# Optimization experiments

Hardware: AMD Instinct MI355X
Metric: run time of the kernel (lower is better)

The kernel has to match this reference:

```python
import jax, jax.numpy as jnp
import numpy as np

N_USER = 100000
N_SELLER = 50000
E = 640000
D_U = 128
D_S = 64
H = 128
B = 50000


def setup_inputs() -> dict:
    key = jax.random.key(0)
    ks = jax.random.split(key, 24)

    def w(k, shape):
        # Glorot-ish scaling by fan_in
        return jax.random.normal(k, shape, dtype=jnp.float32) / np.sqrt(shape[0])

    return {
        "x_user": jax.random.normal(ks[0], (N_USER, D_U), dtype=jnp.float32),
        "x_seller": jax.random.normal(ks[1], (N_SELLER, D_S), dtype=jnp.float32),
        "src_buy": jax.random.randint(ks[2], (E,), 0, N_USER),
        "dst_buy": jax.random.randint(ks[3], (E,), 0, N_SELLER),
        "src_rev": jax.random.randint(ks[4], (E,), 0, N_SELLER),
        "dst_rev": jax.random.randint(ks[5], (E,), 0, N_USER),
        "mask_user": jax.random.randint(ks[6], (B,), 0, N_USER),
        "mask_seller": jax.random.randint(ks[7], (B,), 0, N_SELLER),
        # layer 1: (user,buy,seller) conv: src=user(D_U), dst=seller(D_S)
        "Wl1_buy": w(ks[8], (D_U, H)), "Wr1_buy": w(ks[9], (D_S, H)),
        "b1_buy": jnp.zeros((H,), jnp.float32),
        # layer 1: (seller,bought by,user) conv: src=seller(D_S), dst=user(D_U)
        "Wl1_rev": w(ks[10], (D_S, H)), "Wr1_rev": w(ks[11], (D_U, H)),
        "b1_rev": jnp.zeros((H,), jnp.float32),
        # layer 2 (both node types now have H features)
        "Wl2_buy": w(ks[12], (H, H)), "Wr2_buy": w(ks[13], (H, H)),
        "b2_buy": jnp.zeros((H,), jnp.float32),
        "Wl2_rev": w(ks[14], (H, H)), "Wr2_rev": w(ks[15], (H, H)),
        "b2_rev": jnp.zeros((H,), jnp.float32),
        # final head: Linear(2H, 1)
        "Wlin": w(ks[16], (2 * H, 1)), "blin": jnp.zeros((1,), jnp.float32),
    }


def _sage(x_src, x_dst, src, dst, Wl, Wr, b):
    """PyG SAGEConv: lin_l(mean_j x_src[j]) + lin_r(x_dst); bias on aggr branch."""
    n_dst = x_dst.shape[0]
    agg = jax.ops.segment_sum(x_src[src], dst, num_segments=n_dst)      # [n_dst, d_src]
    cnt = jax.ops.segment_sum(jnp.ones(src.shape, x_src.dtype), dst, num_segments=n_dst)
    mean = agg / jnp.maximum(cnt, 1.0)[:, None]                          # mean aggr, 0 for isolated
    return mean @ Wl + b + x_dst @ Wr


def reference(x_user, x_seller, src_buy, dst_buy, src_rev, dst_rev,
              mask_user, mask_seller,
              Wl1_buy, Wr1_buy, b1_buy, Wl1_rev, Wr1_rev, b1_rev,
              Wl2_buy, Wr2_buy, b2_buy, Wl2_rev, Wr2_rev, b2_rev,
              Wlin, blin):
    # layer 1 (HeteroConv aggr='sum' is trivial: one relation per dst type)
    s1 = jax.nn.relu(_sage(x_user, x_seller, src_buy, dst_buy, Wl1_buy, Wr1_buy, b1_buy))
    u1 = jax.nn.relu(_sage(x_seller, x_user, src_rev, dst_rev, Wl1_rev, Wr1_rev, b1_rev))
    # layer 2
    s2 = jax.nn.relu(_sage(u1, s1, src_buy, dst_buy, Wl2_buy, Wr2_buy, b2_buy))
    u2 = jax.nn.relu(_sage(s1, u1, src_rev, dst_rev, Wl2_rev, Wr2_rev, b2_rev))
    # masked gather + concat + linear + sigmoid
    x = jnp.concatenate((u2[mask_user], s2[mask_seller]), axis=1)        # [B, 2H]
    return jax.nn.sigmoid(x @ Wlin + blin).reshape(-1)
```

## Files before the change

kernel.cpp:

```cpp
#include <hip/hip_runtime.h>

#define N_USER   100000
#define N_SELLER 50000
#define NEDGE    640000
#define DU       128
#define DS       64
#define HH       128
#define BSZ      50000

#define ECHUNK   2048
#define NBLK     313
#define PW       128
#define NPART_B  391
#define NPART_R  782

#define CVT_BLK  15625
#define PREP_BLK 448

#define NB1_BUY  391
#define NB1_REV  782
#define NB2      391

#define AGG1_BUY_BLK 12500
#define AGG1_REV_BLK 25000
#define AGG2_BLK     12500

typedef unsigned short ushort_t;
typedef __attribute__((ext_vector_type(4))) unsigned short u16x4;
typedef __attribute__((ext_vector_type(8))) unsigned short u16x8;
typedef __attribute__((ext_vector_type(8))) short bf16x8;
typedef __attribute__((ext_vector_type(4))) float f32x4;

__device__ __forceinline__ float bf2f(ushort_t u) {
  union { unsigned int i; float f; } v; v.i = ((unsigned int)u) << 16; return v.f;
}
__device__ __forceinline__ ushort_t f2bf(float f) {
  union { float f; unsigned int i; } v; v.f = f;
  unsigned int x = v.i;
  unsigned int r = x + 0x7FFFu + ((x >> 16) & 1u);
  return (ushort_t)(r >> 16);
}

__global__ void __launch_bounds__(256) k_hist_cvt_prep(
    const int* __restrict__ dst_buy, const int* __restrict__ dst_rev,
    int* __restrict__ H_buy, int* __restrict__ H_rev,
    const float* __restrict__ x_user, ushort_t* __restrict__ xu_bf,
    const float* __restrict__ x_seller, ushort_t* __restrict__ xs_bf,
    const float* __restrict__ Wl1b, const float* __restrict__ Wr1b, ushort_t* __restrict__ o1b,
    const float* __restrict__ Wl1r, const float* __restrict__ Wr1r, ushort_t* __restrict__ o1r,
    const float* __restrict__ Wl2b, const float* __restrict__ Wr2b, ushort_t* __restrict__ o2b,
    const float* __restrict__ Wl2r, const float* __restrict__ Wr2r, ushort_t* __restrict__ o2r) {
  __shared__ int lh[NPART_R];
  int b = blockIdx.x;
  int t = threadIdx.x;
  if (b < 2 * NBLK) {
    bool is_buy = b < NBLK;
    int bb = is_buy ? b : b - NBLK;
    const int* dst = is_buy ? dst_buy : dst_rev;
    int* H = is_buy ? H_buy : H_rev;
    int np = is_buy ? NPART_B : NPART_R;
    for (int i = t; i < np; i += 256) lh[i] = 0;
    __syncthreads();
    int base = bb * ECHUNK;
#pragma unroll
    for (int i = 0; i < 8; ++i) {
      int e = base + i * 256 + t;
      if (e < NEDGE) atomicAdd(&lh[dst[e] >> 7], 1);
    }
    __syncthreads();
    for (int p = t; p < np; p += 256) H[p * NBLK + bb] = lh[p];
  } else if (b < 2 * NBLK + CVT_BLK) {
    int idx = (b - 2 * NBLK) * 256 + t;
    const int na4 = N_USER * DU / 4;
    const float* in; ushort_t* out;
    if (idx < na4) { in = x_user + idx * 4; out = xu_bf + idx * 4; }
    else { idx -= na4; in = x_seller + idx * 4; out = xs_bf + idx * 4; }
    float4 v = *(const float4*)in;
    u16x4 r;
    r.x = f2bf(v.x); r.y = f2bf(v.y); r.z = f2bf(v.z); r.w = f2bf(v.w);
    *(u16x4*)out = r;
  } else {
    int idx = (b - 2 * NBLK - CVT_BLK) * 256 + t;
    const float *Wl, *Wr; ushort_t* out; int D1;
    if (idx < 24576)      { Wl = Wl1b; Wr = Wr1b; out = o1b; D1 = 128; }
    else if (idx < 49152) { idx -= 24576; Wl = Wl1r; Wr = Wr1r; out = o1r; D1 = 64; }
    else if (idx < 81920) { idx -= 49152; Wl = Wl2b; Wr = Wr2b; out = o2b; D1 = 128; }
    else                  { idx -= 81920; Wl = Wl2r; Wr = Wr2r; out = o2r; D1 = 128; }
    int f = idx >> 9;
    int r = idx & 511;
    int l = r >> 3;
    int j = r & 7;
    int kcidx = f >> 3;
    int c = f & 7;
    int h = (l & 15) + c * 16;
    int k = kcidx * 32 + (l >> 4) * 8 + j;
    float w = (k < D1) ? Wl[k * HH + h] : Wr[(k - D1) * HH + h];
    out[idx] = f2bf(w);
  }
}

__global__ void __launch_bounds__(256) k_rowscan(
    int* __restrict__ H_buy, int* __restrict__ H_rev,
    int* __restrict__ rowtot_buy, int* __restrict__ rowtot_rev) {
  __shared__ int lds[256];
  int p = blockIdx.x, t = threadIdx.x;
  int* H; int* rowtot; int row;
  if (p < NPART_B) { H = H_buy; rowtot = rowtot_buy; row = p; }
  else             { H = H_rev; rowtot = rowtot_rev; row = p - NPART_B; }
  int i0 = 2 * t, i1 = 2 * t + 1;
  int v0 = (i0 < NBLK) ? H[row * NBLK + i0] : 0;
  int v1 = (i1 < NBLK) ? H[row * NBLK + i1] : 0;
  int tot = v0 + v1;
  lds[t] = tot;
  __syncthreads();
  for (int d = 1; d < 256; d <<= 1) {
    int x = (t >= d) ? lds[t - d] : 0;
    __syncthreads();
    lds[t] += x;
    __syncthreads();
  }
  int excl = lds[t] - tot;
  if (i0 < NBLK) H[row * NBLK + i0] = excl;
  if (i1 < NBLK) H[row * NBLK + i1] = excl + v0;
  if (t == 255) rowtot[row] = lds[255];
}

__global__ void __launch_bounds__(256) k_colscan(
    const int* __restrict__ rowtot_buy, const int* __restrict__ rowtot_rev,
    int* __restrict__ pstart_buy, int* __restrict__ pstart_rev) {
  __shared__ int lds[256];
  const int* rt; int* ps; int n;
  if (blockIdx.x == 0) { rt = rowtot_buy; ps = pstart_buy; n = NPART_B; }
  else                 { rt = rowtot_rev; ps = pstart_rev; n = NPART_R; }
  int t = threadIdx.x;
  int v[4]; int tot = 0;
#pragma unroll
  for (int i = 0; i < 4; ++i) { int idx = t * 4 + i; v[i] = (idx < n) ? rt[idx] : 0; tot += v[i]; }
  lds[t] = tot;
  __syncthreads();
  for (int d = 1; d < 256; d <<= 1) {
    int x = (t >= d) ? lds[t - d] : 0;
    __syncthreads();
    lds[t] += x;
    __syncthreads();
  }
  int excl = lds[t] - tot;
#pragma unroll
  for (int i = 0; i < 4; ++i) {
    int idx = t * 4 + i;
    if (idx < n) { ps[idx] = excl; excl += v[i]; }
  }
  if (t == 255) ps[n] = lds[255];
}

__global__ void __launch_bounds__(256) k_pscat(
    const int* __restrict__ src_buy, const int* __restrict__ dst_buy,
    const int* __restrict__ src_rev, const int* __restrict__ dst_rev,
    const int* __restrict__ H_buy, const int* __restrict__ H_rev,
    const int* __restrict__ pstart_buy, const int* __restrict__ pstart_rev,
    unsigned int* __restrict__ part_buy, unsigned int* __restrict__ part_rev) {
  __shared__ int lc[NPART_R];
  int b = blockIdx.x, t = threadIdx.x;
  bool is_buy = b < NBLK;
  int bb = is_buy ? b : b - NBLK;
  const int* src = is_buy ? src_buy : src_rev;
  const int* dst = is_buy ? dst_buy : dst_rev;
  const int* H   = is_buy ? H_buy : H_rev;
  const int* ps  = is_buy ? pstart_buy : pstart_rev;
  unsigned int* part = is_buy ? part_buy : part_rev;
  int np = is_buy ? NPART_B : NPART_R;
  for (int i = t; i < np; i += 256) lc[i] = 0;
  __syncthreads();
  int base = bb * ECHUNK;
#pragma unroll
  for (int i = 0; i < 8; ++i) {
    int e = base + i * 256 + t;
    if (e < NEDGE) {
      int d = dst[e], s = src[e];
      int p = d >> 7;
      int r = atomicAdd(&lc[p], 1);
      int pos = ps[p] + H[p * NBLK + bb] + r;
      part[pos] = ((unsigned int)(d & (PW - 1)) << 20) | (unsigned int)s;
    }
  }
}

__global__ void __launch_bounds__(256) k_csr(
    const unsigned int* __restrict__ part_buy, const unsigned int* __restrict__ part_rev,
    const int* __restrict__ pstart_buy, const int* __restrict__ pstart_rev,
    int* __restrict__ off_buy, int* __restrict__ off_rev,
    int* __restrict__ csr_buy, int* __restrict__ csr_rev) {
  __shared__ int lcnt[PW], loff[PW], sc[PW];
  int B = blockIdx.x, t = threadIdx.x;
  bool is_buy = B < NPART_B;
  int p = is_buy ? B : B - NPART_B;
  const unsigned int* part = is_buy ? part_buy : part_rev;
  const int* ps = is_buy ? pstart_buy : pstart_rev;
  int* off = is_buy ? off_buy : off_rev;
  int* csr = is_buy ? csr_buy : csr_rev;
  int nnode = is_buy ? N_SELLER : N_USER;
  int s0 = ps[p], s1 = ps[p + 1];
  if (t < PW) lcnt[t] = 0;
  __syncthreads();
  for (int e = s0 + t; e < s1; e += 256) {
    int d = (int)(part[e] >> 20);
    atomicAdd(&lcnt[d], 1);
  }
  __syncthreads();
  int v = (t < PW) ? lcnt[t] : 0;
  if (t < PW) sc[t] = v;
  __syncthreads();
  for (int d = 1; d < PW; d <<= 1) {
    int x = (t >= d && t < PW) ? sc[t - d] : 0;
    __syncthreads();
    if (t < PW) sc[t] += x;
    __syncthreads();
  }
  if (t < PW) {
    loff[t] = sc[t] - v;
    int node = p * PW + t;
    if (node < nnode) off[node] = s0 + loff[t];
    lcnt[t] = 0;
  }
  if (B == 0 && t == 0) { off_buy[N_SELLER] = NEDGE; off_rev[N_USER] = NEDGE; }
  __syncthreads();
  for (int e = s0 + t; e < s1; e += 256) {
    unsigned int pk = part[e];
    int l = (int)(pk >> 20);
    int r = atomicAdd(&lcnt[l], 1);
    csr[s0 + loff[l] + r] = (int)(pk & 0xFFFFFu);
  }
}

template <int D, int U>
__device__ __forceinline__ void agg_body(
    int blk, const ushort_t* __restrict__ X,
    const int* __restrict__ off, const int* __restrict__ csr,
    const int* __restrict__ idxs, int nrows,
    ushort_t* __restrict__ out) {
  constexpr int LPR = D / 8;
  constexpr int EPW = 64 / LPR;
  int wave = threadIdx.x >> 6;
  int lane = threadIdx.x & 63;
  int n = blk * 4 + wave;
  if (n >= nrows) return;
  int node = idxs ? idxs[n] : n;
  int g = lane / LPR;
  int c = (lane % LPR) * 8;
  int i0 = off[node], i1 = off[node + 1];

  float acc[8];
#pragma unroll
  for (int j = 0; j < 8; ++j) acc[j] = 0.f;

  for (int i = i0 + g; i < i1; i += U * EPW) {
    int idx[U];
    u16x8 v[U];
#pragma unroll
    for (int u = 0; u < U; ++u) {
      int ii = i + u * EPW;
      idx[u] = (ii < i1) ? csr[ii] : csr[i];
    }
#pragma unroll
    for (int u = 0; u < U; ++u)
      v[u] = *(const u16x8*)(X + (size_t)idx[u] * D + c);
#pragma unroll
    for (int u = 0; u < U; ++u) {
      if (i + u * EPW < i1) {
#pragma unroll
        for (int j = 0; j < 8; ++j) acc[j] += bf2f(v[u][j]);
      }
    }
  }

#pragma unroll
  for (int mm = LPR; mm < 64; mm <<= 1) {
#pragma unroll
    for (int j = 0; j < 8; ++j) acc[j] += __shfl_xor(acc[j], mm);
  }

  if (g == 0) {
    int deg = i1 - i0;
    float inv = 1.f / (float)(deg > 0 ? deg : 1);
    u16x8 r;
#pragma unroll
    for (int j = 0; j < 8; ++j) r[j] = f2bf(acc[j] * inv);
    *(u16x8*)(out + (size_t)n * D + c) = r;
  }
}

__global__ void __launch_bounds__(256) agg_layer1(
    const ushort_t* __restrict__ xu_bf, const ushort_t* __restrict__ xs_bf,
    const int* __restrict__ off_buy, const int* __restrict__ csr_buy,
    const int* __restrict__ off_rev, const int* __restrict__ csr_rev,
    ushort_t* __restrict__ mean_buy, ushort_t* __restrict__ mean_rev) {
  int b = blockIdx.x;
  if (b < AGG1_BUY_BLK)
    agg_body<128, 4>(b, xu_bf, off_buy, csr_buy, nullptr, N_SELLER, mean_buy);
  else
    agg_body<64, 2>(b - AGG1_BUY_BLK, xs_bf, off_rev, csr_rev, nullptr, N_USER, mean_rev);
}

__global__ void __launch_bounds__(256) agg_layer2(
    const ushort_t* __restrict__ u1, const ushort_t* __restrict__ s1,
    const int* __restrict__ off_buy, const int* __restrict__ csr_buy,
    const int* __restrict__ off_rev, const int* __restrict__ csr_rev,
    const int* __restrict__ mask_seller, const int* __restrict__ mask_user,
    ushort_t* __restrict__ mean_buy, ushort_t* __restrict__ mean_rev) {
  int b = blockIdx.x;
  if (b < AGG2_BLK)
    agg_body<128, 4>(b, u1, off_buy, csr_buy, mask_seller, BSZ, mean_buy);
  else
    agg_body<128, 4>(b - AGG2_BLK, s1, off_rev, csr_rev, mask_user, BSZ, mean_rev);
}

template <int K, bool HEAD>
__device__ __forceinline__ void gemm_body(
    int blk, ushort_t* lds,
    const ushort_t* __restrict__ A1, int ld1, int D1, const int* __restrict__ mask1,
    const ushort_t* __restrict__ A2, int ld2, const int* __restrict__ mask2,
    const ushort_t* __restrict__ Wf, const float* __restrict__ bias,
    ushort_t* __restrict__ out, float* __restrict__ partial,
    const float* __restrict__ wlin_seg, int M) {
  constexpr int NCH = K / 32;
  int t = threadIdx.x;
  int wave = t >> 6;
  int lane = t & 63;

  constexpr int ITERS = (HH * K * 2) / 4096;
#pragma unroll
  for (int i = 0; i < ITERS; ++i) {
    const ushort_t* g = Wf + i * 2048 + t * 8;
    ushort_t* l = lds + i * 2048 + wave * 512;
    __builtin_amdgcn_global_load_lds((const __attribute__((address_space(1))) void*)g,
                                     (__attribute__((address_space(3))) void*)l, 16, 0, 0);
  }

  int row0 = blk * 128 + wave * 32;
  int kb = (lane >> 4) << 3;
  bf16x8 af[2][NCH];
#pragma unroll
  for (int s = 0; s < 2; ++s) {
    int r = row0 + s * 16 + (lane & 15);
    int rsafe = r < M ? r : M - 1;
    int a1 = mask1 ? mask1[rsafe] : rsafe;
    int a2 = mask2 ? mask2[rsafe] : rsafe;
#pragma unroll
    for (int kc = 0; kc < NCH; ++kc) {
      int k = kc * 32 + kb;
      const ushort_t* ap = (k < D1) ? (A1 + (size_t)a1 * ld1 + k)
                                    : (A2 + (size_t)a2 * ld2 + (k - D1));
      af[s][kc] = *(const bf16x8*)ap;
    }
  }

  f32x4 acc[2][8];
#pragma unroll
  for (int s = 0; s < 2; ++s)
#pragma unroll
    for (int c = 0; c < 8; ++c) acc[s][c] = (f32x4){0.f, 0.f, 0.f, 0.f};

  __syncthreads();

#pragma unroll
  for (int kc = 0; kc < NCH; ++kc) {
#pragma unroll
    for (int c = 0; c < 8; ++c) {
      bf16x8 bf = *(const bf16x8*)(lds + ((kc * 8 + c) * 512 + lane * 8));
      acc[0][c] = __builtin_amdgcn_mfma_f32_16x16x32_bf16(af[0][kc], bf, acc[0][c], 0, 0, 0);
      acc[1][c] = __builtin_amdgcn_mfma_f32_16x16x32_bf16(af[1][kc], bf, acc[1][c], 0, 0, 0);
    }
  }

  int colb = lane & 15;
  if constexpr (!HEAD) {
#pragma unroll
    for (int s = 0; s < 2; ++s) {
      int rbase = row0 + s * 16 + ((lane >> 4) << 2);
#pragma unroll
      for (int c = 0; c < 8; ++c) {
        int col = c * 16 + colb;
        float bv = bias[col];
#pragma unroll
        for (int j = 0; j < 4; ++j) {
          int rout = rbase + j;
          if (rout < M) {
            float v = fmaxf(acc[s][c][j] + bv, 0.f);
            out[(size_t)rout * HH + col] = f2bf(v);
          }
        }
      }
    }
  } else {
    float wl[8], bv[8];
#pragma unroll
    for (int c = 0; c < 8; ++c) {
      wl[c] = wlin_seg[c * 16 + colb];
      bv[c] = bias[c * 16 + colb];
    }
#pragma unroll
    for (int s = 0; s < 2; ++s) {
      float p0 = 0.f, p1 = 0.f, p2 = 0.f, p3 = 0.f;
#pragma unroll
      for (int c = 0; c < 8; ++c) {
        p0 += fmaxf(acc[s][c][0] + bv[c], 0.f) * wl[c];
        p1 += fmaxf(acc[s][c][1] + bv[c], 0.f) * wl[c];
        p2 += fmaxf(acc[s][c][2] + bv[c], 0.f) * wl[c];
        p3 += fmaxf(acc[s][c][3] + bv[c], 0.f) * wl[c];
      }
#pragma unroll
      for (int m = 1; m < 16; m <<= 1) {
        p0 += __shfl_xor(p0, m);
        p1 += __shfl_xor(p1, m);
        p2 += __shfl_xor(p2, m);
        p3 += __shfl_xor(p3, m);
      }
      if (colb == 0) {
        int rbase = row0 + s * 16 + ((lane >> 4) << 2);
        if (rbase + 0 < M) partial[rbase + 0] = p0;
        if (rbase + 1 < M) partial[rbase + 1] = p1;
        if (rbase + 2 < M) partial[rbase + 2] = p2;
        if (rbase + 3 < M) partial[rbase + 3] = p3;
      }
    }
  }
}

__global__ void __launch_bounds__(256) gemm_layer1(
    const ushort_t* __restrict__ mean_buy, const ushort_t* __restrict__ xs_bf,
    const ushort_t* __restrict__ mean_rev, const ushort_t* __restrict__ xu_bf,
    const ushort_t* __restrict__ wt1_buy, const float* __restrict__ b1_buy,
    const ushort_t* __restrict__ wt1_rev, const float* __restrict__ b1_rev,
    ushort_t* __restrict__ s1, ushort_t* __restrict__ u1) {
  __shared__ ushort_t lds[HH * 192];
  int b = blockIdx.x;
  if (b < NB1_BUY)
    gemm_body<192, false>(b, lds, mean_buy, 128, 128, nullptr, xs_bf, 64, nullptr,
                          wt1_buy, b1_buy, s1, nullptr, nullptr, N_SELLER);
  else
    gemm_body<192, false>(b - NB1_BUY, lds, mean_rev, 64, 64, nullptr, xu_bf, 128, nullptr,
                          wt1_rev, b1_rev, u1, nullptr, nullptr, N_USER);
}

__global__ void __launch_bounds__(256) gemm_layer2(
    const ushort_t* __restrict__ mean_buy, const ushort_t* __restrict__ s1,
    const ushort_t* __restrict__ mean_rev, const ushort_t* __restrict__ u1,
    const int* __restrict__ mask_seller, const int* __restrict__ mask_user,
    const ushort_t* __restrict__ wt2_buy, const float* __restrict__ b2_buy,
    const ushort_t* __restrict__ wt2_rev, const float* __restrict__ b2_rev,
    const float* __restrict__ wlin,
    float* __restrict__ ps, float* __restrict__ pu) {
  __shared__ ushort_t lds[HH * 256];
  int b = blockIdx.x;
  if (b < NB2)
    gemm_body<256, true>(b, lds, mean_buy, 128, 128, nullptr, s1, 128, mask_seller,
                         wt2_buy, b2_buy, nullptr, ps, wlin + 128, BSZ);
  else
    gemm_body<256, true>(b - NB2, lds, mean_rev, 128, 128, nullptr, u1, 128, mask_user,
                         wt2_rev, b2_rev, nullptr, pu, wlin, BSZ);
}

__global__ void head_fin(const float* __restrict__ pu, const float* __restrict__ ps,
                         const float* __restrict__ blin, float* __restrict__ out) {
  int i = blockIdx.x * 256 + threadIdx.x;
  if (i < BSZ) {
    float z = pu[i] + ps[i] + blin[0];
    out[i] = 1.f / (1.f + expf(-z));
  }
}

extern "C" void kernel_launch(void* const* d_in, const int* in_sizes, int n_in,
                              void* d_out, int out_size, void* d_ws, size_t ws_size,
                              hipStream_t stream) {
  const float* x_user    = (const float*)d_in[0];
  const float* x_seller  = (const float*)d_in[1];
  const int* src_buy  = (const int*)d_in[2];
  const int* dst_buy  = (const int*)d_in[3];
  const int* src_rev  = (const int*)d_in[4];
  const int* dst_rev  = (const int*)d_in[5];
  const int* mask_user   = (const int*)d_in[6];
  const int* mask_seller = (const int*)d_in[7];
  const float* Wl1_buy = (const float*)d_in[8];
  const float* Wr1_buy = (const float*)d_in[9];
  const float* b1_buy  = (const float*)d_in[10];
  const float* Wl1_rev = (const float*)d_in[11];
  const float* Wr1_rev = (const float*)d_in[12];
  const float* b1_rev  = (const float*)d_in[13];
  const float* Wl2_buy = (const float*)d_in[14];
  const float* Wr2_buy = (const float*)d_in[15];
  const float* b2_buy  = (const float*)d_in[16];
  const float* Wl2_rev = (const float*)d_in[17];
  const float* Wr2_rev = (const float*)d_in[18];
  const float* b2_rev  = (const float*)d_in[19];
  const float* Wlin    = (const float*)d_in[20];
  const float* blin    = (const float*)d_in[21];

  char* ws = (char*)d_ws;
  size_t o = 0;
  auto alloc = [&](size_t bytes) { size_t p = o; o += (bytes + 255) & ~(size_t)255; return p; };
  size_t wt1_buy_o = alloc(HH * 192 * 2);
  size_t wt1_rev_o = alloc(HH * 192 * 2);
  size_t wt2_buy_o = alloc(HH * 256 * 2);
  size_t wt2_rev_o = alloc(HH * 256 * 2);
  size_t H_buy_o = alloc((size_t)NPART_B * NBLK * 4);
  size_t H_rev_o = alloc((size_t)NPART_R * NBLK * 4);
  size_t rowtot_buy_o = alloc(NPART_B * 4);
  size_t rowtot_rev_o = alloc(NPART_R * 4);
  size_t pstart_buy_o = alloc((NPART_B + 1) * 4);
  size_t pstart_rev_o = alloc((NPART_R + 1) * 4);
  size_t part_buy_o = alloc((size_t)NEDGE * 4);
  size_t part_rev_o = alloc((size_t)NEDGE * 4);
  size_t off_buy_o = alloc((size_t)(N_SELLER + 1) * 4);
  size_t off_rev_o = alloc((size_t)(N_USER + 1) * 4);
  size_t csr_buy_o = alloc((size_t)NEDGE * 4);
  size_t csr_rev_o = alloc((size_t)NEDGE * 4);
  size_t xu_bf_o = alloc((size_t)N_USER * DU * 2);
  size_t xs_bf_o = alloc((size_t)N_SELLER * DS * 2);
  size_t mean_buy_o = alloc((size_t)N_SELLER * 128 * 2);
  size_t mean_rev_o = alloc((size_t)N_USER * 64 * 2);
  size_t s1_o = alloc((size_t)N_SELLER * HH * 2);
  size_t u1_o = alloc((size_t)N_USER * HH * 2);
  size_t ps_o = alloc((size_t)50048 * 4);
  size_t pu_o = alloc((size_t)50048 * 4);
  (void)ws_size;

  ushort_t* wt1_buy = (ushort_t*)(ws + wt1_buy_o);
  ushort_t* wt1_rev = (ushort_t*)(ws + wt1_rev_o);
  ushort_t* wt2_buy = (ushort_t*)(ws + wt2_buy_o);
  ushort_t* wt2_rev = (ushort_t*)(ws + wt2_rev_o);
  int* H_buy = (int*)(ws + H_buy_o);
  int* H_rev = (int*)(ws + H_rev_o);
  int* rowtot_buy = (int*)(ws + rowtot_buy_o);
  int* rowtot_rev = (int*)(ws + rowtot_rev_o);
  int* pstart_buy = (int*)(ws + pstart_buy_o);
  int* pstart_rev = (int*)(ws + pstart_rev_o);
  unsigned int* part_buy = (unsigned int*)(ws + part_buy_o);
  unsigned int* part_rev = (unsigned int*)(ws + part_rev_o);
  int* off_buy = (int*)(ws + off_buy_o);
  int* off_rev = (int*)(ws + off_rev_o);
  int* csr_buy = (int*)(ws + csr_buy_o);
  int* csr_rev = (int*)(ws + csr_rev_o);
  ushort_t* xu_bf = (ushort_t*)(ws + xu_bf_o);
  ushort_t* xs_bf = (ushort_t*)(ws + xs_bf_o);
  ushort_t* mean_buy = (ushort_t*)(ws + mean_buy_o);
  ushort_t* mean_rev = (ushort_t*)(ws + mean_rev_o);
  ushort_t* s1 = (ushort_t*)(ws + s1_o);
  ushort_t* u1 = (ushort_t*)(ws + u1_o);
  float* ps = (float*)(ws + ps_o);
  float* pu = (float*)(ws + pu_o);

  k_hist_cvt_prep<<<2 * NBLK + CVT_BLK + PREP_BLK, 256, 0, stream>>>(
      dst_buy, dst_rev, H_buy, H_rev,
      x_user, xu_bf, x_seller, xs_bf,
      Wl1_buy, Wr1_buy, wt1_buy, Wl1_rev, Wr1_rev, wt1_rev,
      Wl2_buy, Wr2_buy, wt2_buy, Wl2_rev, Wr2_rev, wt2_rev);
  k_rowscan<<<NPART_B + NPART_R, 256, 0, stream>>>(H_buy, H_rev, rowtot_buy, rowtot_rev);
  k_colscan<<<2, 256, 0, stream>>>(rowtot_buy, rowtot_rev, pstart_buy, pstart_rev);
  k_pscat<<<2 * NBLK, 256, 0, stream>>>(src_buy, dst_buy, src_rev, dst_rev,
                                        H_buy, H_rev, pstart_buy, pstart_rev,
                                        part_buy, part_rev);
  k_csr<<<NPART_B + NPART_R, 256, 0, stream>>>(part_buy, part_rev, pstart_buy, pstart_rev,
                                               off_buy, off_rev, csr_buy, csr_rev);

  agg_layer1<<<AGG1_BUY_BLK + AGG1_REV_BLK, 256, 0, stream>>>(
      xu_bf, xs_bf, off_buy, csr_buy, off_rev, csr_rev, mean_buy, mean_rev);
  gemm_layer1<<<NB1_BUY + NB1_REV, 256, 0, stream>>>(
      mean_buy, xs_bf, mean_rev, xu_bf, wt1_buy, b1_buy, wt1_rev, b1_rev, s1, u1);

  agg_layer2<<<AGG2_BLK + AGG2_BLK, 256, 0, stream>>>(
      u1, s1, off_buy, csr_buy, off_rev, csr_rev, mask_seller, mask_user,
      mean_buy, mean_rev);
  gemm_layer2<<<NB2 + NB2, 256, 0, stream>>>(
      mean_buy, s1, mean_rev, u1, mask_seller, mask_user,
      wt2_buy, b2_buy, wt2_rev, b2_rev, Wlin, ps, pu);

  head_fin<<<(BSZ + 255) / 256, 256, 0, stream>>>(pu, ps, blin, (float*)d_out);
}
```

Measured before the change: 202.6 us.

## Move feature conversion into scatter kernel and streamline gather-mean aggregation loop

The bf16 conversion of node features and the weight re-layout now run inside the scatter kernel rather than the histogram kernel, so the histogram kernel is small and the heavy conversion work overlaps the scatter phase. The aggregation loop now runs full unrolled chunks without per-edge predicates and handles leftover edges in a separate tail loop. It unpacks bf16 pairs with bit masks into float2 accumulators. The unroll factor for the 128-wide aggregations drops from 4 to 2, which may reduce memory-level parallelism in the gathers while lowering register use.

Measured after the change: 203.3 us, median of 2. No clear change (+0.3%).

```diff
diff --git a/kernel.cpp b/kernel.cpp
--- a/kernel.cpp
+++ b/kernel.cpp
@@ -40,35 +40,123 @@
   unsigned int r = x + 0x7FFFu + ((x >> 16) & 1u);
   return (ushort_t)(r >> 16);
 }
-
-__global__ void __launch_bounds__(256) k_hist_cvt_prep(
+__device__ __forceinline__ float u2f(unsigned int u) {
+  union { unsigned int i; float f; } v; v.i = u; return v.f;
+}
+
+__global__ void __launch_bounds__(256) k_hist(
     const int* __restrict__ dst_buy, const int* __restrict__ dst_rev,
+    int* __restrict__ H_buy, int* __restrict__ H_rev) {
+  __shared__ int lh[NPART_R];
+  int b = blockIdx.x, t = threadIdx.x;
+  bool is_buy = b < NBLK;
+  int bb = is_buy ? b : b - NBLK;
+  const int* dst = is_buy ? dst_buy : dst_rev;
+  int* H = is_buy ? H_buy : H_rev;
+  int np = is_buy ? NPART_B : NPART_R;
+  for (int i = t; i < np; i += 256) lh[i] = 0;
+  __syncthreads();
+  int base = bb * ECHUNK;
+#pragma unroll
+  for (int i = 0; i < 8; ++i) {
+    int e = base + i * 256 + t;
+    if (e < NEDGE) atomicAdd(&lh[dst[e] >> 7], 1);
+  }
+  __syncthreads();
+  for (int p = t; p < np; p += 256) H[p * NBLK + bb] = lh[p];
+}
+
+__global__ void __launch_bounds__(256) k_rowscan(
     int* __restrict__ H_buy, int* __restrict__ H_rev,
+    int* __restrict__ rowtot_buy, int* __restrict__ rowtot_rev) {
+  __shared__ int lds[256];
+  int p = blockIdx.x, t = threadIdx.x;
+  int* H; int* rowtot; int row;
+  if (p < NPART_B) { H = H_buy; rowtot = rowtot_buy; row = p; }
+  else             { H = H_rev; rowtot = rowtot_rev; row = p - NPART_B; }
+  int i0 = 2 * t, i1 = 2 * t + 1;
+  int v0 = (i0 < NBLK) ? H[row * NBLK + i0] : 0;
+  int v1 = (i1 < NBLK) ? H[row * NBLK + i1] : 0;
+  int tot = v0 + v1;
+  lds[t] = tot;
+  __syncthreads();
+  for (int d = 1; d < 256; d <<= 1) {
+    int x = (t >= d) ? lds[t - d] : 0;
+    __syncthreads();
+    lds[t] += x;
+    __syncthreads();
+  }
+  int excl = lds[t] - tot;
+  if (i0 < NBLK) H[row * NBLK + i0] = excl;
+  if (i1 < NBLK) H[row * NBLK + i1] = excl + v0;
+  if (t == 255) rowtot[row] = lds[255];
+}
+
+__global__ void __launch_bounds__(256) k_colscan(
+    const int* __restrict__ rowtot_buy, const int* __restrict__ rowtot_rev,
+    int* __restrict__ pstart_buy, int* __restrict__ pstart_rev) {
+  __shared__ int lds[256];
+  const int* rt; int* ps; int n;
+  if (blockIdx.x == 0) { rt = rowtot_buy; ps = pstart_buy; n = NPART_B; }
+  else                 { rt = rowtot_rev; ps = pstart_rev; n = NPART_R; }
+  int t = threadIdx.x;
+  int v[4]; int tot = 0;
+#pragma unroll
+  for (int i = 0; i < 4; ++i) { int idx = t * 4 + i; v[i] = (idx < n) ? rt[idx] : 0; tot += v[i]; }
+  lds[t] = tot;
+  __syncthreads();
+  for (int d = 1; d < 256; d <<= 1) {
+    int x = (t >= d) ? lds[t - d] : 0;
+    __syncthreads();
+    lds[t] += x;
+    __syncthreads();
+  }
+  int excl = lds[t] - tot;
+#pragma unroll
+  for (int i = 0; i < 4; ++i) {
+    int idx = t * 4 + i;
+    if (idx < n) { ps[idx] = excl; excl += v[i]; }
+  }
+  if (t == 255) ps[n] = lds[255];
+}
+
+__global__ void __launch_bounds__(256) k_scat_cvt_prep(
+    const int* __restrict__ src_buy, const int* __restrict__ dst_buy,
+    const int* __restrict__ src_rev, const int* __restrict__ dst_rev,
+    const int* __restrict__ H_buy, const int* __restrict__ H_rev,
+    const int* __restrict__ pstart_buy, const int* __restrict__ pstart_rev,
+    unsigned int* __restrict__ part_buy, unsigned int* __restrict__ part_rev,
     const float* __restrict__ x_user, ushort_t* __restrict__ xu_bf,
     const float* __restrict__ x_seller, ushort_t* __restrict__ xs_bf,
     const float* __restrict__ Wl1b, const float* __restrict__ Wr1b, ushort_t* __restrict__ o1b,
     const float* __restrict__ Wl1r, const float* __restrict__ Wr1r, ushort_t* __restrict__ o1r,
     const float* __restrict__ Wl2b, const float* __restrict__ Wr2b, ushort_t* __restrict__ o2b,
     const float* __restrict__ Wl2r, const float* __restrict__ Wr2r, ushort_t* __restrict__ o2r) {
-  __shared__ int lh[NPART_R];
-  int b = blockIdx.x;
-  int t = threadIdx.x;
+  __shared__ int lc[NPART_R];
+  int b = blockIdx.x, t = threadIdx.x;
   if (b < 2 * NBLK) {
     bool is_buy = b < NBLK;
     int bb = is_buy ? b : b - NBLK;
+    const int* src = is_buy ? src_buy : src_rev;
     const int* dst = is_buy ? dst_buy : dst_rev;
-    int* H = is_buy ? H_buy : H_rev;
+    const int* H   = is_buy ? H_buy : H_rev;
+    const int* ps  = is_buy ? pstart_buy : pstart_rev;
+    unsigned int* part = is_buy ? part_buy : part_rev;
     int np = is_buy ? NPART_B : NPART_R;
-    for (int i = t; i < np; i += 256) lh[i] = 0;
+    for (int i = t; i < np; i += 256) lc[i] = 0;
     __syncthreads();
     int base = bb * ECHUNK;
 #pragma unroll
     for (int i = 0; i < 8; ++i) {
       int e = base + i * 256 + t;
-      if (e < NEDGE) atomicAdd(&lh[dst[e] >> 7], 1);
-    }
-    __syncthreads();
-    for (int p = t; p < np; p += 256) H[p * NBLK + bb] = lh[p];
+      if (e < NEDGE) {
+        int d = dst[e], s = src[e];
+        int p = d >> 7;
+        int r = atomicAdd(&lc[p], 1);
+        int pos = ps[p] + H[p * NBLK + bb] + r;
+        part[pos] = ((unsigned int)(d & (PW - 1)) << 20) | (unsigned int)s;
+      }
+    }
   } else if (b < 2 * NBLK + CVT_BLK) {
     int idx = (b - 2 * NBLK) * 256 + t;
     const int na4 = N_USER * DU / 4;
@@ -99,92 +187,6 @@
   }
 }
 
-__global__ void __launch_bounds__(256) k_rowscan(
-    int* __restrict__ H_buy, int* __restrict__ H_rev,
-    int* __restrict__ rowtot_buy, int* __restrict__ rowtot_rev) {
-  __shared__ int lds[256];
-  int p = blockIdx.x, t = threadIdx.x;
-  int* H; int* rowtot; int row;
-  if (p < NPART_B) { H = H_buy; rowtot = rowtot_buy; row = p; }
-  else             { H = H_rev; rowtot = rowtot_rev; row = p - NPART_B; }
-  int i0 = 2 * t, i1 = 2 * t + 1;
-  int v0 = (i0 < NBLK) ? H[row * NBLK + i0] : 0;
-  int v1 = (i1 < NBLK) ? H[row * NBLK + i1] : 0;
-  int tot = v0 + v1;
-  lds[t] = tot;
-  __syncthreads();
-  for (int d = 1; d < 256; d <<= 1) {
-    int x = (t >= d) ? lds[t - d] : 0;
-    __syncthreads();
-    lds[t] += x;
-    __syncthreads();
-  }
-  int excl = lds[t] - tot;
-  if (i0 < NBLK) H[row * NBLK + i0] = excl;
-  if (i1 < NBLK) H[row * NBLK + i1] = excl + v0;
-  if (t == 255) rowtot[row] = lds[255];
-}
-
-__global__ void __launch_bounds__(256) k_colscan(
-    const int* __restrict__ rowtot_buy, const int* __restrict__ rowtot_rev,
-    int* __restrict__ pstart_buy, int* __restrict__ pstart_rev) {
-  __shared__ int lds[256];
-  const int* rt; int* ps; int n;
-  if (blockIdx.x == 0) { rt = rowtot_buy; ps = pstart_buy; n = NPART_B; }
-  else                 { rt = rowtot_rev; ps = pstart_rev; n = NPART_R; }
-  int t = threadIdx.x;
-  int v[4]; int tot = 0;
-#pragma unroll
-  for (int i = 0; i < 4; ++i) { int idx = t * 4 + i; v[i] = (idx < n) ? rt[idx] : 0; tot += v[i]; }
-  lds[t] = tot;
-  __syncthreads();
-  for (int d = 1; d < 256; d <<= 1) {
-    int x = (t >= d) ? lds[t - d] : 0;
-    __syncthreads();
-    lds[t] += x;
-    __syncthreads();
-  }
-  int excl = lds[t] - tot;
-#pragma unroll
-  for (int i = 0; i < 4; ++i) {
-    int idx = t * 4 + i;
-    if (idx < n) { ps[idx] = excl; excl += v[i]; }
-  }
-  if (t == 255) ps[n] = lds[255];
-}
-
-__global__ void __launch_bounds__(256) k_pscat(
-    const int* __restrict__ src_buy, const int* __restrict__ dst_buy,
-    const int* __restrict__ src_rev, const int* __restrict__ dst_rev,
-    const int* __restrict__ H_buy, const int* __restrict__ H_rev,
-    const int* __restrict__ pstart_buy, const int* __restrict__ pstart_rev,
-    unsigned int* __restrict__ part_buy, unsigned int* __restrict__ part_rev) {
-  __shared__ int lc[NPART_R];
-  int b = blockIdx.x, t = threadIdx.x;
-  bool is_buy = b < NBLK;
-  int bb = is_buy ? b : b - NBLK;
-  const int* src = is_buy ? src_buy : src_rev;
-  const int* dst = is_buy ? dst_buy : dst_rev;
-  const int* H   = is_buy ? H_buy : H_rev;
-  const int* ps  = is_buy ? pstart_buy : pstart_rev;
-  unsigned int* part = is_buy ? part_buy : part_rev;
-  int np = is_buy ? NPART_B : NPART_R;
-  for (int i = t; i < np; i += 256) lc[i] = 0;
-  __syncthreads();
-  int base = bb * ECHUNK;
-#pragma unroll
-  for (int i = 0; i < 8; ++i) {
-    int e = base + i * 256 + t;
-    if (e < NEDGE) {
-      int d = dst[e], s = src[e];
-      int p = d >> 7;
-      int r = atomicAdd(&lc[p], 1);
-      int pos = ps[p] + H[p * NBLK + bb] + r;
-      part[pos] = ((unsigned int)(d & (PW - 1)) << 20) | (unsigned int)s;
-    }
-  }
-}
-
 __global__ void __launch_bounds__(256) k_csr(
     const unsigned int* __restrict__ part_buy, const unsigned int* __restrict__ part_rev,
     const int* __restrict__ pstart_buy, const int* __restrict__ pstart_rev,
@@ -248,35 +250,45 @@
   int g = lane / LPR;
   int c = (lane % LPR) * 8;
   int i0 = off[node], i1 = off[node + 1];
-
-  float acc[8];
-#pragma unroll
-  for (int j = 0; j < 8; ++j) acc[j] = 0.f;
-
-  for (int i = i0 + g; i < i1; i += U * EPW) {
-    int idx[U];
-    u16x8 v[U];
+  const ushort_t* Xc = X + c;
+
+  float2 acc[4];
+#pragma unroll
+  for (int q = 0; q < 4; ++q) acc[q] = (float2){0.f, 0.f};
+
+  int i = i0 + g;
+  for (; i + (U - 1) * EPW < i1; i += U * EPW) {
+    int idxv[U];
+#pragma unroll
+    for (int u = 0; u < U; ++u) idxv[u] = csr[i + u * EPW];
+    uint4 v[U];
+#pragma unroll
+    for (int u = 0; u < U; ++u)
+      v[u] = *(const uint4*)(Xc + (size_t)idxv[u] * D);
 #pragma unroll
     for (int u = 0; u < U; ++u) {
-      int ii = i + u * EPW;
-      idx[u] = (ii < i1) ? csr[ii] : csr[i];
-    }
-#pragma unroll
-    for (int u = 0; u < U; ++u)
-      v[u] = *(const u16x8*)(X + (size_t)idx[u] * D + c);
-#pragma unroll
-    for (int u = 0; u < U; ++u) {
-      if (i + u * EPW < i1) {
-#pragma unroll
-        for (int j = 0; j < 8; ++j) acc[j] += bf2f(v[u][j]);
-      }
-    }
+      acc[0] += (float2){u2f(v[u].x << 16), u2f(v[u].x & 0xFFFF0000u)};
+      acc[1] += (float2){u2f(v[u].y << 16), u2f(v[u].y & 0xFFFF0000u)};
+      acc[2] += (float2){u2f(v[u].z << 16), u2f(v[u].z & 0xFFFF0000u)};
+      acc[3] += (float2){u2f(v[u].w << 16), u2f(v[u].w & 0xFFFF0000u)};
+    }
+  }
+  for (; i < i1; i += EPW) {
+    int s = csr[i];
+    uint4 v = *(const uint4*)(Xc + (size_t)s * D);
+    acc[0] += (float2){u2f(v.x << 16), u2f(v.x & 0xFFFF0000u)};
+    acc[1] += (float2){u2f(v.y << 16), u2f(v.y & 0xFFFF0000u)};
+    acc[2] += (float2){u2f(v.z << 16), u2f(v.z & 0xFFFF0000u)};
+    acc[3] += (float2){u2f(v.w << 16), u2f(v.w & 0xFFFF0000u)};
   }
 
 #pragma unroll
   for (int mm = LPR; mm < 64; mm <<= 1) {
 #pragma unroll
-    for (int j = 0; j < 8; ++j) acc[j] += __shfl_xor(acc[j], mm);
+    for (int q = 0; q < 4; ++q) {
+      acc[q].x += __shfl_xor(acc[q].x, mm);
+      acc[q].y += __shfl_xor(acc[q].y, mm);
+    }
   }
 
   if (g == 0) {
@@ -284,7 +296,10 @@
     float inv = 1.f / (float)(deg > 0 ? deg : 1);
     u16x8 r;
 #pragma unroll
-    for (int j = 0; j < 8; ++j) r[j] = f2bf(acc[j] * inv);
+    for (int q = 0; q < 4; ++q) {
+      r[2 * q]     = f2bf(acc[q].x * inv);
+      r[2 * q + 1] = f2bf(acc[q].y * inv);
+    }
     *(u16x8*)(out + (size_t)n * D + c) = r;
   }
 }
@@ -296,7 +311,7 @@
     ushort_t* __restrict__ mean_buy, ushort_t* __restrict__ mean_rev) {
   int b = blockIdx.x;
   if (b < AGG1_BUY_BLK)
-    agg_body<128, 4>(b, xu_bf, off_buy, csr_buy, nullptr, N_SELLER, mean_buy);
+    agg_body<128, 2>(b, xu_bf, off_buy, csr_buy, nullptr, N_SELLER, mean_buy);
   else
     agg_body<64, 2>(b - AGG1_BUY_BLK, xs_bf, off_rev, csr_rev, nullptr, N_USER, mean_rev);
 }
@@ -309,9 +324,9 @@
     ushort_t* __restrict__ mean_buy, ushort_t* __restrict__ mean_rev) {
   int b = blockIdx.x;
   if (b < AGG2_BLK)
-    agg_body<128, 4>(b, u1, off_buy, csr_buy, mask_seller, BSZ, mean_buy);
+    agg_body<128, 2>(b, u1, off_buy, csr_buy, mask_seller, BSZ, mean_buy);
   else
-    agg_body<128, 4>(b - AGG2_BLK, s1, off_rev, csr_rev, mask_user, BSZ, mean_rev);
+    agg_body<128, 2>(b - AGG2_BLK, s1, off_rev, csr_rev, mask_user, BSZ, mean_rev);
 }
 
 template <int K, bool HEAD>
@@ -549,16 +564,15 @@
   float* ps = (float*)(ws + ps_o);
   float* pu = (float*)(ws + pu_o);
 
-  k_hist_cvt_prep<<<2 * NBLK + CVT_BLK + PREP_BLK, 256, 0, stream>>>(
-      dst_buy, dst_rev, H_buy, H_rev,
+  k_hist<<<2 * NBLK, 256, 0, stream>>>(dst_buy, dst_rev, H_buy, H_rev);
+  k_rowscan<<<NPART_B + NPART_R, 256, 0, stream>>>(H_buy, H_rev, rowtot_buy, rowtot_rev);
+  k_colscan<<<2, 256, 0, stream>>>(rowtot_buy, rowtot_rev, pstart_buy, pstart_rev);
+  k_scat_cvt_prep<<<2 * NBLK + CVT_BLK + PREP_BLK, 256, 0, stream>>>(
+      src_buy, dst_buy, src_rev, dst_rev, H_buy, H_rev, pstart_buy, pstart_rev,
+      part_buy, part_rev,
       x_user, xu_bf, x_seller, xs_bf,
       Wl1_buy, Wr1_buy, wt1_buy, Wl1_rev, Wr1_rev, wt1_rev,
       Wl2_buy, Wr2_buy, wt2_buy, Wl2_rev, Wr2_rev, wt2_rev);
-  k_rowscan<<<NPART_B + NPART_R, 256, 0, stream>>>(H_buy, H_rev, rowtot_buy, rowtot_rev);
-  k_colscan<<<2, 256, 0, stream>>>(rowtot_buy, rowtot_rev, pstart_buy, pstart_rev);
-  k_pscat<<<2 * NBLK, 256, 0, stream>>>(src_buy, dst_buy, src_rev, dst_rev,
-                                        H_buy, H_rev, pstart_buy, pstart_rev,
-                                        part_buy, part_rev);
   k_csr<<<NPART_B + NPART_R, 256, 0, stream>>>(part_buy, part_rev, pstart_buy, pstart_rev,
                                                off_buy, off_rev, csr_buy, csr_rev);
 
```
